# Optimization experiments

Measured on AMD Instinct MI355X. Metric: run time of the kernel, lower is better.

## Reference

```python
import jax, jax.numpy as jnp
import numpy as np

L, B, S, D = 12, 2, 2048, 768
QK, H, V = 128, 512, 32000
SCALE = 128 ** (-0.5)


def setup_inputs() -> dict:
    key = jax.random.key(0)
    ks = jax.random.split(key, 11)
    p = lambda k, shp: jax.random.normal(k, shp, dtype=jnp.float32) * 0.02
    return {
        "layer_outputs": jax.random.normal(ks[0], (L, B, S, D), dtype=jnp.float32),
        "Wq": p(ks[1], (D, QK)), "bq": jnp.zeros((QK,), jnp.float32),
        "Wk": p(ks[2], (D, QK)), "bk": jnp.zeros((QK,), jnp.float32),
        "Wv": p(ks[3], (D, H)),  "bv": jnp.zeros((H,), jnp.float32),
        "W1": p(ks[4], (H, H // 2)), "b1": jnp.zeros((H // 2,), jnp.float32),
        "W2": p(ks[5], (H // 2, V)), "b2": jnp.zeros((V,), jnp.float32),
    }


def reference(layer_outputs, Wq, bq, Wk, bk, Wv, bv, W1, b1, W2, b2):
    # layer_outputs: (L, B, S, D) -> h: (S, L, B, D) as in torch permute(2,0,1,3)
    h = jnp.transpose(layer_outputs, (2, 0, 1, 3))
    q_in = h.mean(axis=1)                              # (S, B, D)
    q = jax.nn.relu(q_in @ Wq + bq)                    # (S, B, 128)
    k = jax.nn.relu(h @ Wk + bk)                       # (S, L, B, 128)
    scores = jnp.einsum('sbd,slbd->slb', q, k)[..., None] * SCALE  # (S, L, B, 1)
    attn = jax.nn.softmax(scores, axis=1)              # softmax over layer axis
    v = h @ Wv + bv                                    # (S, L, B, H)
    agg = jnp.sum(attn * v, axis=1)                    # (S, B, H)
    agg = jnp.transpose(agg, (1, 0, 2))                # (B, S, H)
    mid = jax.nn.relu(agg @ W1 + b1)                   # (B, S, H//2); dropout is eval-mode identity
    return mid @ W2 + b2                               # (B, S, V)
```

## Files before the change

kernel.cpp:

```cpp
#include <hip/hip_runtime.h>

#define Snum 2048
#define SCALE 0.08838834764831845f

typedef __attribute__((ext_vector_type(8))) __bf16 bf16x8;
typedef __attribute__((ext_vector_type(4))) float f32x4;

__device__ inline unsigned short f2bf(float f) {
    unsigned int u = __float_as_uint(f);
    unsigned int r = u + 0x7FFFu + ((u >> 16) & 1u);
    return (unsigned short)(r >> 16);
}
__device__ inline float bf2f(unsigned short u) {
    return __uint_as_float(((unsigned)u) << 16);
}
__device__ inline void gld_lds16(const unsigned short* g, unsigned short* l) {
    __builtin_amdgcn_global_load_lds(
        (const __attribute__((address_space(1))) unsigned int*)g,
        (__attribute__((address_space(3))) unsigned int*)l, 16, 0, 0);
}

__global__ __launch_bounds__(256) void transpose_small(
    const float* __restrict__ Wv, unsigned short* __restrict__ Wvt,
    const float* __restrict__ W1, unsigned short* __restrict__ W1t,
    const float* __restrict__ Wk, const float* __restrict__ Wq,
    unsigned short* __restrict__ Wqkt)
{
    __shared__ float t[32][33];
    const int id = blockIdx.x;
    const float* in; unsigned short* out; int K, N, bx, by;
    if (id < 384)      { int q = id;       in = Wv; out = Wvt;  K = 768; N = 512; bx = q & 15; by = q >> 4; }
    else if (id < 512) { int q = id - 384; in = W1; out = W1t;  K = 512; N = 256; bx = q & 7;  by = q >> 3; }
    else if (id < 608) { int q = id - 512; in = Wk; out = Wqkt; K = 768; N = 128; bx = q & 3;  by = q >> 2; }
    else               { int q = id - 608; in = Wq; out = Wqkt + (size_t)128 * 768; K = 768; N = 128; bx = q & 3; by = q >> 2; }

    const int tx = threadIdx.x & 31, ty = threadIdx.x >> 5;
    #pragma unroll
    for (int i = 0; i < 4; ++i) {
        int k = by * 32 + ty + i * 8, n = bx * 32 + tx;
        t[ty + i * 8][tx] = in[(size_t)k * N + n];
    }
    __syncthreads();
    #pragma unroll
    for (int i = 0; i < 4; ++i) {
        int n = bx * 32 + ty + i * 8, k = by * 32 + tx;
        out[(size_t)n * K + k] = f2bf(t[tx][ty + i * 8]);
    }
}

__global__ __launch_bounds__(512) void proj_qk(
    const float* __restrict__ x, const unsigned short* __restrict__ Bt,
    const float* __restrict__ bk,
    unsigned short* __restrict__ Kall,
    unsigned short* __restrict__ Pq)
{
    __shared__ __align__(16) unsigned short As[2][128 * 32];
    __shared__ __align__(16) unsigned short Bs[2][256 * 32];
    const int tid = threadIdx.x;
    const int wid = tid >> 6, lane = tid & 63;
    const int wm = (wid >> 2) * 64, wn = (wid & 3) * 64;
    const int lr = lane & 15, g = lane >> 4;
    const int r0 = blockIdx.x * 128;
    const int K = 768, NT = 24;

    const int arow = tid >> 2, akc = (tid & 3) * 8;

    f32x4 acc[4][4] = {};

    float4 a0 = *(const float4*)(x + (size_t)(r0 + arow) * K + akc);
    float4 a1 = *(const float4*)(x + (size_t)(r0 + arow) * K + akc + 4);
    {
        unsigned short v[8];
        v[0] = f2bf(a0.x); v[1] = f2bf(a0.y); v[2] = f2bf(a0.z); v[3] = f2bf(a0.w);
        v[4] = f2bf(a1.x); v[5] = f2bf(a1.y); v[6] = f2bf(a1.z); v[7] = f2bf(a1.w);
        *(uint4*)&As[0][arow * 32 + akc] = *(uint4*)v;
    }
    #pragma unroll
    for (int c = 0; c < 2; ++c) {
        int rr = wid * 32 + c * 16;
        gld_lds16(Bt + (size_t)(rr + (lane >> 2)) * K + (lane & 3) * 8, &Bs[0][rr * 32]);
    }
    __syncthreads();

    for (int t = 0; t < NT; ++t) {
        const int cur = t & 1, nxt = cur ^ 1;
        if (t + 1 < NT) {
            const int k0 = (t + 1) * 32;
            a0 = *(const float4*)(x + (size_t)(r0 + arow) * K + k0 + akc);
            a1 = *(const float4*)(x + (size_t)(r0 + arow) * K + k0 + akc + 4);
            #pragma unroll
            for (int c = 0; c < 2; ++c) {
                int rr = wid * 32 + c * 16;
                gld_lds16(Bt + (size_t)(rr + (lane >> 2)) * K + k0 + (lane & 3) * 8,
                          &Bs[nxt][rr * 32]);
            }
        }

        bf16x8 aF[4], bF[4];
        #pragma unroll
        for (int mm = 0; mm < 4; ++mm) aF[mm] = *(const bf16x8*)&As[cur][(wm + mm * 16 + lr) * 32 + g * 8];
        #pragma unroll
        for (int nn = 0; nn < 4; ++nn) bF[nn] = *(const bf16x8*)&Bs[cur][(wn + nn * 16 + lr) * 32 + g * 8];
        #pragma unroll
        for (int mm = 0; mm < 4; ++mm)
            #pragma unroll
            for (int nn = 0; nn < 4; ++nn)
                acc[mm][nn] = __builtin_amdgcn_mfma_f32_16x16x32_bf16(bF[nn], aF[mm], acc[mm][nn], 0, 0, 0);

        if (t + 1 < NT) {
            unsigned short v[8];
            v[0] = f2bf(a0.x); v[1] = f2bf(a0.y); v[2] = f2bf(a0.z); v[3] = f2bf(a0.w);
            v[4] = f2bf(a1.x); v[5] = f2bf(a1.y); v[6] = f2bf(a1.z); v[7] = f2bf(a1.w);
            *(uint4*)&As[nxt][arow * 32 + akc] = *(uint4*)v;
        }
        __syncthreads();
    }

    #pragma unroll
    for (int mm = 0; mm < 4; ++mm)
        #pragma unroll
        for (int nn = 0; nn < 4; ++nn) {
            const int row = r0 + wm + mm * 16 + lr;
            const int colb = wn + nn * 16 + g * 4;
            unsigned short o[4];
            if (colb < 128) {
                #pragma unroll
                for (int reg = 0; reg < 4; ++reg) {
                    float kv = acc[mm][nn][reg] + bk[colb + reg];
                    o[reg] = f2bf(kv > 0.f ? kv : 0.f);
                }
                *(ushort4*)&Kall[(size_t)row * 128 + colb] = *(ushort4*)o;
            } else {
                #pragma unroll
                for (int reg = 0; reg < 4; ++reg) o[reg] = f2bf(acc[mm][nn][reg]);
                *(ushort4*)&Pq[(size_t)row * 128 + (colb - 128)] = *(ushort4*)o;
            }
        }
}

__global__ __launch_bounds__(256) void scores_plus_w2t(
    const float* __restrict__ x,
    const unsigned short* __restrict__ Pq,
    const float* __restrict__ bq,
    const unsigned short* __restrict__ Kall,
    unsigned short* __restrict__ hbar,
    const float* __restrict__ W2, unsigned short* __restrict__ W2t)
{
    if (blockIdx.x >= 1024) {
        __shared__ float t[32][33];
        const int id = blockIdx.x - 1024;
        const int bx = id >> 3, by = id & 7;
        const int tx = threadIdx.x & 31, ty = threadIdx.x >> 5;
        #pragma unroll
        for (int i = 0; i < 4; ++i) {
            int k = by * 32 + ty + i * 8, n = bx * 32 + tx;
            t[ty + i * 8][tx] = W2[(size_t)k * 32000 + n];
        }
        __syncthreads();
        #pragma unroll
        for (int i = 0; i < 4; ++i) {
            int n = bx * 32 + ty + i * 8, k = by * 32 + tx;
            W2t[(size_t)n * 256 + k] = f2bf(t[tx][ty + i * 8]);
        }
        return;
    }

    const int wid = threadIdx.x >> 6, lane = threadIdx.x & 63;
    const int r = blockIdx.x * 4 + wid;
    const int b = r >> 11, s = r & 2047;

    float qa = 0.f, qb_ = 0.f;
    #pragma unroll
    for (int l = 0; l < 12; ++l) {
        const unsigned short* prow = Pq + ((size_t)(l * 2 + b) * Snum + s) * 128 + lane * 2;
        unsigned int u = *(const unsigned int*)prow;
        qa += bf2f((unsigned short)(u & 0xFFFF));
        qb_ += bf2f((unsigned short)(u >> 16));
    }
    float q0 = qa * (1.0f / 12.0f) + bq[lane * 2];
    float q1 = qb_ * (1.0f / 12.0f) + bq[lane * 2 + 1];
    q0 = q0 > 0.f ? q0 : 0.f;
    q1 = q1 > 0.f ? q1 : 0.f;
    q0 = bf2f(f2bf(q0)); q1 = bf2f(f2bf(q1));

    float sc[12];
    #pragma unroll
    for (int l = 0; l < 12; ++l) {
        const unsigned short* krow = Kall + ((size_t)(l * 2 + b) * Snum + s) * 128 + lane * 2;
        unsigned int u = *(const unsigned int*)krow;
        float p = q0 * bf2f((unsigned short)(u & 0xFFFF)) + q1 * bf2f((unsigned short)(u >> 16));
        #pragma unroll
        for (int off = 32; off > 0; off >>= 1) p += __shfl_xor(p, off, 64);
        sc[l] = p * SCALE;
    }
    float m = sc[0];
    #pragma unroll
    for (int l = 1; l < 12; ++l) m = fmaxf(m, sc[l]);
    float att[12], den = 0.f;
    #pragma unroll
    for (int l = 0; l < 12; ++l) { att[l] = __expf(sc[l] - m); den += att[l]; }
    const float inv = 1.0f / den;
    #pragma unroll
    for (int l = 0; l < 12; ++l) att[l] *= inv;

    #pragma unroll
    for (int jv = 0; jv < 3; ++jv) {
        const int d0 = jv * 256 + lane * 4;
        float a0 = 0.f, a1 = 0.f, a2 = 0.f, a3 = 0.f;
        #pragma unroll
        for (int l = 0; l < 12; ++l) {
            const float4 v = *(const float4*)(x + ((size_t)(l * 2 + b) * Snum + s) * 768 + d0);
            a0 += att[l] * v.x; a1 += att[l] * v.y; a2 += att[l] * v.z; a3 += att[l] * v.w;
        }
        ushort4 o;
        o.x = f2bf(a0); o.y = f2bf(a1); o.z = f2bf(a2); o.w = f2bf(a3);
        *(ushort4*)(hbar + (size_t)r * 768 + d0) = o;
    }
}

template <int RELU, int OUT_BF16>
__global__ __launch_bounds__(256) void gemm64(
    const unsigned short* __restrict__ A, const unsigned short* __restrict__ Bt,
    const float* __restrict__ bias, void* __restrict__ out, int M, int N, int K)
{
    __shared__ __align__(16) unsigned short As[64][40];
    __shared__ __align__(16) unsigned short Bs[64][40];
    const int tid = threadIdx.x;
    const int bn = blockIdx.x, bm = blockIdx.y;
    const int wid = tid >> 6, lane = tid & 63;
    const int wm = (wid >> 1) * 32, wn = (wid & 1) * 32;
    const int lr = lane & 15, g = lane >> 4;
    const int r0 = bm * 64, c0 = bn * 64;

    f32x4 acc[2][2] = {};
    const int row = tid >> 2, kc = (tid & 3) * 8;

    for (int k0 = 0; k0 < K; k0 += 32) {
        __syncthreads();
        *(uint4*)&As[row][kc] = *(const uint4*)(A  + (size_t)(r0 + row) * K + k0 + kc);
        *(uint4*)&Bs[row][kc] = *(const uint4*)(Bt + (size_t)(c0 + row) * K + k0 + kc);
        __syncthreads();

        bf16x8 aF[2], bF[2];
        #pragma unroll
        for (int mm = 0; mm < 2; ++mm) aF[mm] = *(const bf16x8*)&As[wm + mm * 16 + lr][g * 8];
        #pragma unroll
        for (int nn = 0; nn < 2; ++nn) bF[nn] = *(const bf16x8*)&Bs[wn + nn * 16 + lr][g * 8];
        #pragma unroll
        for (int mm = 0; mm < 2; ++mm)
            #pragma unroll
            for (int nn = 0; nn < 2; ++nn)
                acc[mm][nn] = __builtin_amdgcn_mfma_f32_16x16x32_bf16(bF[nn], aF[mm], acc[mm][nn], 0, 0, 0);
    }

    #pragma unroll
    for (int mm = 0; mm < 2; ++mm)
        #pragma unroll
        for (int nn = 0; nn < 2; ++nn) {
            const int orow = r0 + wm + mm * 16 + lr;
            const int colb = c0 + wn + nn * 16 + g * 4;
            float vr[4];
            #pragma unroll
            for (int reg = 0; reg < 4; ++reg) {
                float v = acc[mm][nn][reg] + bias[colb + reg];
                vr[reg] = (RELU && v < 0.f) ? 0.f : v;
            }
            if (OUT_BF16) {
                unsigned short o[4];
                #pragma unroll
                for (int reg = 0; reg < 4; ++reg) o[reg] = f2bf(vr[reg]);
                *(ushort4*)&((unsigned short*)out)[(size_t)orow * N + colb] = *(ushort4*)o;
            } else {
                *(float4*)&((float*)out)[(size_t)orow * N + colb] = *(float4*)vr;
            }
        }
}

__global__ __launch_bounds__(256) void gemm_out(
    const unsigned short* __restrict__ A,
    const unsigned short* __restrict__ Bt,
    const float* __restrict__ bias, float* __restrict__ out)
{
    __shared__ __align__(16) unsigned short As[2][128 * 32];
    __shared__ __align__(16) unsigned short Bs[2][128 * 32];
    const int K = 256, N = 32000, NT = 8;
    const int orig = blockIdx.x;
    const int swz = (orig & 7) * 1000 + (orig >> 3);
    const int bn = swz >> 5, bm = swz & 31;
    const int tid = threadIdx.x;
    const int wid = tid >> 6, lane = tid & 63;
    const int wm = (wid >> 1) * 64, wn = (wid & 1) * 64;
    const int lr = lane & 15, g = lane >> 4;
    const int r0 = bm * 128, c0 = bn * 128;

    f32x4 acc[4][4] = {};

    #pragma unroll
    for (int c = 0; c < 2; ++c) {
        int rr = wid * 32 + c * 16;
        gld_lds16(A  + (size_t)(r0 + rr + (lane >> 2)) * K + (lane & 3) * 8, &As[0][rr * 32]);
        gld_lds16(Bt + (size_t)(c0 + rr + (lane >> 2)) * K + (lane & 3) * 8, &Bs[0][rr * 32]);
    }
    __syncthreads();

    for (int t = 0; t < NT; ++t) {
        const int cur = t & 1, nxt = cur ^ 1;
        if (t + 1 < NT) {
            const int k0 = (t + 1) * 32;
            #pragma unroll
            for (int c = 0; c < 2; ++c) {
                int rr = wid * 32 + c * 16;
                gld_lds16(A  + (size_t)(r0 + rr + (lane >> 2)) * K + k0 + (lane & 3) * 8, &As[nxt][rr * 32]);
                gld_lds16(Bt + (size_t)(c0 + rr + (lane >> 2)) * K + k0 + (lane & 3) * 8, &Bs[nxt][rr * 32]);
            }
        }

        bf16x8 aF[4], bF[4];
        #pragma unroll
        for (int mm = 0; mm < 4; ++mm) aF[mm] = *(const bf16x8*)&As[cur][(wm + mm * 16 + lr) * 32 + g * 8];
        #pragma unroll
        for (int nn = 0; nn < 4; ++nn) bF[nn] = *(const bf16x8*)&Bs[cur][(wn + nn * 16 + lr) * 32 + g * 8];
        #pragma unroll
        for (int mm = 0; mm < 4; ++mm)
            #pragma unroll
            for (int nn = 0; nn < 4; ++nn)
                acc[mm][nn] = __builtin_amdgcn_mfma_f32_16x16x32_bf16(bF[nn], aF[mm], acc[mm][nn], 0, 0, 0);
        __syncthreads();
    }

    #pragma unroll
    for (int mm = 0; mm < 4; ++mm)
        #pragma unroll
        for (int nn = 0; nn < 4; ++nn) {
            const int row = r0 + wm + mm * 16 + lr;
            const int colb = c0 + wn + nn * 16 + g * 4;
            const float4 b4 = *(const float4*)&bias[colb];
            f32x4 o = acc[mm][nn];
            o[0] += b4.x; o[1] += b4.y; o[2] += b4.z; o[3] += b4.w;
            __builtin_nontemporal_store(o, (f32x4*)&out[(size_t)row * N + colb]);
        }
}

extern "C" void kernel_launch(void* const* d_in, const int* in_sizes, int n_in,
                              void* d_out, int out_size, void* d_ws, size_t ws_size,
                              hipStream_t stream) {
    (void)in_sizes; (void)n_in; (void)out_size; (void)ws_size;

    const float* x  = (const float*)d_in[0];
    const float* Wq = (const float*)d_in[1];
    const float* bq = (const float*)d_in[2];
    const float* Wk = (const float*)d_in[3];
    const float* bk = (const float*)d_in[4];
    const float* Wv = (const float*)d_in[5];
    const float* bv = (const float*)d_in[6];
    const float* W1 = (const float*)d_in[7];
    const float* b1 = (const float*)d_in[8];
    const float* W2 = (const float*)d_in[9];
    const float* b2 = (const float*)d_in[10];

    char* p = (char*)d_ws;
    unsigned short* Wqkt  = (unsigned short*)p; p += (size_t)256 * 768 * 2;
    unsigned short* Wvt   = (unsigned short*)p; p += (size_t)512 * 768 * 2;
    unsigned short* W1t   = (unsigned short*)p; p += (size_t)256 * 512 * 2;
    unsigned short* W2t   = (unsigned short*)p; p += (size_t)32000 * 256 * 2;
    unsigned short* Kall  = (unsigned short*)p; p += (size_t)49152 * 128 * 2;
    unsigned short* Pq    = (unsigned short*)p; p += (size_t)49152 * 128 * 2;
    unsigned short* hbar  = (unsigned short*)p; p += (size_t)4096 * 768 * 2;
    unsigned short* aggb  = (unsigned short*)p; p += (size_t)4096 * 512 * 2;
    unsigned short* midb  = (unsigned short*)p; p += (size_t)4096 * 256 * 2;

    transpose_small<<<dim3(704), dim3(256), 0, stream>>>(Wv, Wvt, W1, W1t, Wk, Wq, Wqkt);

    proj_qk<<<dim3(49152 / 128), dim3(512), 0, stream>>>(x, Wqkt, bk, Kall, Pq);

    scores_plus_w2t<<<dim3(1024 + 8000), dim3(256), 0, stream>>>(
        x, Pq, bq, Kall, hbar, W2, W2t);

    gemm64<0, 1><<<dim3(512 / 64, 4096 / 64), dim3(256), 0, stream>>>(
        hbar, Wvt, bv, aggb, 4096, 512, 768);

    gemm64<1, 1><<<dim3(256 / 64, 4096 / 64), dim3(256), 0, stream>>>(
        aggb, W1t, b1, midb, 4096, 256, 512);

    gemm_out<<<dim3(8000), dim3(256), 0, stream>>>(midb, W2t, b2, (float*)d_out);
}
```

Before: 281.7 us.

## Fold Wv into W1 by precomputing combined weight and bias, shrink proj_qk tiles

Because there is no nonlinearity between the value projection and the first MLP layer, the change precomputes G = Wv·W1 (transposed, bf16) with a small GEMM and a combined bias bv·W1 + b1. The two per-token GEMMs (hbar→agg→mid) become one GEMM hbar×G, which removes the aggb intermediate and one launch. gemm64 now uses double-buffered direct global-to-LDS loads, and proj_qk moves to 64-row tiles with 256 threads for more blocks. The combined weight is rounded to bf16 once, which changes numerics slightly, and the extra prep launches run on every call.

```diff
diff --git a/kernel.cpp b/kernel.cpp
--- a/kernel.cpp
+++ b/kernel.cpp
@@ -20,18 +20,25 @@
         (__attribute__((address_space(3))) unsigned int*)l, 16, 0, 0);
 }
 
-__global__ __launch_bounds__(256) void transpose_small(
-    const float* __restrict__ Wv, unsigned short* __restrict__ Wvt,
+__global__ __launch_bounds__(256) void prep_weights(
+    const float* __restrict__ Wv, unsigned short* __restrict__ Wvbf,
     const float* __restrict__ W1, unsigned short* __restrict__ W1t,
     const float* __restrict__ Wk, const float* __restrict__ Wq,
     unsigned short* __restrict__ Wqkt)
 {
+    const int id = blockIdx.x;
+    if (id < 384) {
+        const int base = (id * 256 + threadIdx.x) * 4;
+        const float4 v = *(const float4*)(Wv + base);
+        ushort4 o;
+        o.x = f2bf(v.x); o.y = f2bf(v.y); o.z = f2bf(v.z); o.w = f2bf(v.w);
+        *(ushort4*)(Wvbf + base) = o;
+        return;
+    }
     __shared__ float t[32][33];
-    const int id = blockIdx.x;
     const float* in; unsigned short* out; int K, N, bx, by;
-    if (id < 384)      { int q = id;       in = Wv; out = Wvt;  K = 768; N = 512; bx = q & 15; by = q >> 4; }
-    else if (id < 512) { int q = id - 384; in = W1; out = W1t;  K = 512; N = 256; bx = q & 7;  by = q >> 3; }
-    else if (id < 608) { int q = id - 512; in = Wk; out = Wqkt; K = 768; N = 128; bx = q & 3;  by = q >> 2; }
+    if (id < 512)      { int q = id - 384; in = W1; out = W1t;  K = 512; N = 256; bx = q & 7; by = q >> 3; }
+    else if (id < 608) { int q = id - 512; in = Wk; out = Wqkt; K = 768; N = 128; bx = q & 3; by = q >> 2; }
     else               { int q = id - 608; in = Wq; out = Wqkt + (size_t)128 * 768; K = 768; N = 128; bx = q & 3; by = q >> 2; }
 
     const int tx = threadIdx.x & 31, ty = threadIdx.x >> 5;
@@ -48,19 +55,35 @@
     }
 }
 
-__global__ __launch_bounds__(512) void proj_qk(
+__global__ __launch_bounds__(256) void bias_prime(
+    const unsigned short* __restrict__ W1t, const float* __restrict__ bv,
+    const float* __restrict__ b1, float* __restrict__ bp)
+{
+    const int n = threadIdx.x;
+    float s = b1[n];
+    const unsigned short* row = W1t + (size_t)n * 512;
+    for (int h = 0; h < 512; h += 8) {
+        uint4 u = *(const uint4*)(row + h);
+        const unsigned short* v = (const unsigned short*)&u;
+        #pragma unroll
+        for (int i = 0; i < 8; ++i) s += bv[h + i] * bf2f(v[i]);
+    }
+    bp[n] = s;
+}
+
+__global__ __launch_bounds__(256) void proj_qk(
     const float* __restrict__ x, const unsigned short* __restrict__ Bt,
     const float* __restrict__ bk,
     unsigned short* __restrict__ Kall,
     unsigned short* __restrict__ Pq)
 {
-    __shared__ __align__(16) unsigned short As[2][128 * 32];
+    __shared__ __align__(16) unsigned short As[2][64 * 32];
     __shared__ __align__(16) unsigned short Bs[2][256 * 32];
     const int tid = threadIdx.x;
     const int wid = tid >> 6, lane = tid & 63;
-    const int wm = (wid >> 2) * 64, wn = (wid & 3) * 64;
+    const int wn = wid * 64;
     const int lr = lane & 15, g = lane >> 4;
-    const int r0 = blockIdx.x * 128;
+    const int r0 = blockIdx.x * 64;
     const int K = 768, NT = 24;
 
     const int arow = tid >> 2, akc = (tid & 3) * 8;
@@ -76,8 +99,8 @@
         *(uint4*)&As[0][arow * 32 + akc] = *(uint4*)v;
     }
     #pragma unroll
-    for (int c = 0; c < 2; ++c) {
-        int rr = wid * 32 + c * 16;
+    for (int c = 0; c < 4; ++c) {
+        const int rr = wid * 64 + c * 16;
         gld_lds16(Bt + (size_t)(rr + (lane >> 2)) * K + (lane & 3) * 8, &Bs[0][rr * 32]);
     }
     __syncthreads();
@@ -89,8 +112,8 @@
             a0 = *(const float4*)(x + (size_t)(r0 + arow) * K + k0 + akc);
             a1 = *(const float4*)(x + (size_t)(r0 + arow) * K + k0 + akc + 4);
             #pragma unroll
-            for (int c = 0; c < 2; ++c) {
-                int rr = wid * 32 + c * 16;
+            for (int c = 0; c < 4; ++c) {
+                const int rr = wid * 64 + c * 16;
                 gld_lds16(Bt + (size_t)(rr + (lane >> 2)) * K + k0 + (lane & 3) * 8,
                           &Bs[nxt][rr * 32]);
             }
@@ -98,7 +121,7 @@
 
         bf16x8 aF[4], bF[4];
         #pragma unroll
-        for (int mm = 0; mm < 4; ++mm) aF[mm] = *(const bf16x8*)&As[cur][(wm + mm * 16 + lr) * 32 + g * 8];
+        for (int mm = 0; mm < 4; ++mm) aF[mm] = *(const bf16x8*)&As[cur][(mm * 16 + lr) * 32 + g * 8];
         #pragma unroll
         for (int nn = 0; nn < 4; ++nn) bF[nn] = *(const bf16x8*)&Bs[cur][(wn + nn * 16 + lr) * 32 + g * 8];
         #pragma unroll
@@ -120,7 +143,7 @@
     for (int mm = 0; mm < 4; ++mm)
         #pragma unroll
         for (int nn = 0; nn < 4; ++nn) {
-            const int row = r0 + wm + mm * 16 + lr;
+            const int row = r0 + mm * 16 + lr;
             const int colb = wn + nn * 16 + g * 4;
             unsigned short o[4];
             if (colb < 128) {
@@ -218,39 +241,48 @@
     }
 }
 
-template <int RELU, int OUT_BF16>
+template <int RELU, int OUT_BF16, int BIAS>
 __global__ __launch_bounds__(256) void gemm64(
     const unsigned short* __restrict__ A, const unsigned short* __restrict__ Bt,
     const float* __restrict__ bias, void* __restrict__ out, int M, int N, int K)
 {
-    __shared__ __align__(16) unsigned short As[64][40];
-    __shared__ __align__(16) unsigned short Bs[64][40];
+    __shared__ __align__(16) unsigned short As[2][64 * 32];
+    __shared__ __align__(16) unsigned short Bs[2][64 * 32];
     const int tid = threadIdx.x;
     const int bn = blockIdx.x, bm = blockIdx.y;
     const int wid = tid >> 6, lane = tid & 63;
     const int wm = (wid >> 1) * 32, wn = (wid & 1) * 32;
     const int lr = lane & 15, g = lane >> 4;
     const int r0 = bm * 64, c0 = bn * 64;
+    const int NT = K / 32;
+
+    const int srow = lane >> 2, skc = (lane & 3) * 8;
 
     f32x4 acc[2][2] = {};
-    const int row = tid >> 2, kc = (tid & 3) * 8;
-
-    for (int k0 = 0; k0 < K; k0 += 32) {
-        __syncthreads();
-        *(uint4*)&As[row][kc] = *(const uint4*)(A  + (size_t)(r0 + row) * K + k0 + kc);
-        *(uint4*)&Bs[row][kc] = *(const uint4*)(Bt + (size_t)(c0 + row) * K + k0 + kc);
-        __syncthreads();
+
+    gld_lds16(A  + (size_t)(r0 + wid * 16 + srow) * K + skc, &As[0][wid * 16 * 32]);
+    gld_lds16(Bt + (size_t)(c0 + wid * 16 + srow) * K + skc, &Bs[0][wid * 16 * 32]);
+    __syncthreads();
+
+    for (int t = 0; t < NT; ++t) {
+        const int cur = t & 1, nxt = cur ^ 1;
+        if (t + 1 < NT) {
+            const int k0 = (t + 1) * 32;
+            gld_lds16(A  + (size_t)(r0 + wid * 16 + srow) * K + k0 + skc, &As[nxt][wid * 16 * 32]);
+            gld_lds16(Bt + (size_t)(c0 + wid * 16 + srow) * K + k0 + skc, &Bs[nxt][wid * 16 * 32]);
+        }
 
         bf16x8 aF[2], bF[2];
         #pragma unroll
-        for (int mm = 0; mm < 2; ++mm) aF[mm] = *(const bf16x8*)&As[wm + mm * 16 + lr][g * 8];
-        #pragma unroll
-        for (int nn = 0; nn < 2; ++nn) bF[nn] = *(const bf16x8*)&Bs[wn + nn * 16 + lr][g * 8];
+        for (int mm = 0; mm < 2; ++mm) aF[mm] = *(const bf16x8*)&As[cur][(wm + mm * 16 + lr) * 32 + g * 8];
+        #pragma unroll
+        for (int nn = 0; nn < 2; ++nn) bF[nn] = *(const bf16x8*)&Bs[cur][(wn + nn * 16 + lr) * 32 + g * 8];
         #pragma unroll
         for (int mm = 0; mm < 2; ++mm)
             #pragma unroll
             for (int nn = 0; nn < 2; ++nn)
                 acc[mm][nn] = __builtin_amdgcn_mfma_f32_16x16x32_bf16(bF[nn], aF[mm], acc[mm][nn], 0, 0, 0);
+        __syncthreads();
     }
 
     #pragma unroll
@@ -262,7 +294,7 @@
             float vr[4];
             #pragma unroll
             for (int reg = 0; reg < 4; ++reg) {
-                float v = acc[mm][nn][reg] + bias[colb + reg];
+                float v = acc[mm][nn][reg] + (BIAS ? bias[colb + reg] : 0.f);
                 vr[reg] = (RELU && v < 0.f) ? 0.f : v;
             }
             if (OUT_BF16) {
@@ -297,7 +329,7 @@
 
     #pragma unroll
     for (int c = 0; c < 2; ++c) {
-        int rr = wid * 32 + c * 16;
+        const int rr = wid * 32 + c * 16;
         gld_lds16(A  + (size_t)(r0 + rr + (lane >> 2)) * K + (lane & 3) * 8, &As[0][rr * 32]);
         gld_lds16(Bt + (size_t)(c0 + rr + (lane >> 2)) * K + (lane & 3) * 8, &Bs[0][rr * 32]);
     }
@@ -309,7 +341,7 @@
             const int k0 = (t + 1) * 32;
             #pragma unroll
             for (int c = 0; c < 2; ++c) {
-                int rr = wid * 32 + c * 16;
+                const int rr = wid * 32 + c * 16;
                 gld_lds16(A  + (size_t)(r0 + rr + (lane >> 2)) * K + k0 + (lane & 3) * 8, &As[nxt][rr * 32]);
                 gld_lds16(Bt + (size_t)(c0 + rr + (lane >> 2)) * K + k0 + (lane & 3) * 8, &Bs[nxt][rr * 32]);
             }
@@ -360,27 +392,30 @@
 
     char* p = (char*)d_ws;
     unsigned short* Wqkt  = (unsigned short*)p; p += (size_t)256 * 768 * 2;
-    unsigned short* Wvt   = (unsigned short*)p; p += (size_t)512 * 768 * 2;
+    unsigned short* Wvbf  = (unsigned short*)p; p += (size_t)768 * 512 * 2;
     unsigned short* W1t   = (unsigned short*)p; p += (size_t)256 * 512 * 2;
+    unsigned short* Gtb   = (unsigned short*)p; p += (size_t)256 * 768 * 2;
+    float*          bprim = (float*)p;          p += (size_t)256 * 4;
     unsigned short* W2t   = (unsigned short*)p; p += (size_t)32000 * 256 * 2;
     unsigned short* Kall  = (unsigned short*)p; p += (size_t)49152 * 128 * 2;
     unsigned short* Pq    = (unsigned short*)p; p += (size_t)49152 * 128 * 2;
     unsigned short* hbar  = (unsigned short*)p; p += (size_t)4096 * 768 * 2;
-    unsigned short* aggb  = (unsigned short*)p; p += (size_t)4096 * 512 * 2;
     unsigned short* midb  = (unsigned short*)p; p += (size_t)4096 * 256 * 2;
 
-    transpose_small<<<dim3(704), dim3(256), 0, stream>>>(Wv, Wvt, W1, W1t, Wk, Wq, Wqkt);
-
-    proj_qk<<<dim3(49152 / 128), dim3(512), 0, stream>>>(x, Wqkt, bk, Kall, Pq);
+    prep_weights<<<dim3(704), dim3(256), 0, stream>>>(Wv, Wvbf, W1, W1t, Wk, Wq, Wqkt);
+
+    bias_prime<<<dim3(1), dim3(256), 0, stream>>>(W1t, bv, b1, bprim);
+
+    gemm64<0, 1, 0><<<dim3(768 / 64, 256 / 64), dim3(256), 0, stream>>>(
+        W1t, Wvbf, nullptr, Gtb, 256, 768, 512);
+
+    proj_qk<<<dim3(49152 / 64), dim3(256), 0, stream>>>(x, Wqkt, bk, Kall, Pq);
 
     scores_plus_w2t<<<dim3(1024 + 8000), dim3(256), 0, stream>>>(
         x, Pq, bq, Kall, hbar, W2, W2t);
 
-    gemm64<0, 1><<<dim3(512 / 64, 4096 / 64), dim3(256), 0, stream>>>(
-        hbar, Wvt, bv, aggb, 4096, 512, 768);
-
-    gemm64<1, 1><<<dim3(256 / 64, 4096 / 64), dim3(256), 0, stream>>>(
-        aggb, W1t, b1, midb, 4096, 256, 512);
+    gemm64<1, 1, 1><<<dim3(256 / 64, 4096 / 64), dim3(256), 0, stream>>>(
+        hbar, Gtb, bprim, midb, 4096, 256, 768);
 
     gemm_out<<<dim3(8000), dim3(256), 0, stream>>>(midb, W2t, b2, (float*)d_out);
 }
```

Measured after the change: 286.6 us. No clear change (+1.7%).
